# Performance work log

Measured on AMD Instinct MI355X. Metric: run time of the kernel, lower is better.

Reference implementation:

```python
import jax, jax.numpy as jnp
import numpy as np

N = 8192      # nodes
IN_FEATS = 128
OUT_FEATS = 64
DEG = 16      # avg degree for random edges
NEG_SLOPE = 0.01  # nn.LeakyReLU default


def setup_inputs() -> dict:
    key = jax.random.key(0)
    k1, k2, k3, k4, k5, k6 = jax.random.split(key, 6)
    inputs = jax.random.normal(k1, (N, IN_FEATS), dtype=jnp.float32)
    # Random symmetric adjacency with self-loops (dense, as in the original module)
    us = jax.random.randint(k2, (N * DEG,), 0, N)
    vs = jax.random.randint(k3, (N * DEG,), 0, N)
    A = jnp.zeros((N, N), dtype=jnp.float32)
    A = A.at[us, vs].set(1.0)
    A = A.at[vs, us].set(1.0)
    idx = jnp.arange(N)
    A = A.at[idx, idx].set(1.0)
    # Linear layer params (torch nn.Linear: weight [out, in])
    W = jax.random.normal(k4, (OUT_FEATS, IN_FEATS), dtype=jnp.float32) * (1.0 / np.sqrt(IN_FEATS))
    b = jnp.zeros((OUT_FEATS,), dtype=jnp.float32)
    # attention params, torch.rand -> uniform [0,1)
    a1 = jax.random.uniform(k5, (1, OUT_FEATS), dtype=jnp.float32)
    a2 = jax.random.uniform(k6, (1, OUT_FEATS), dtype=jnp.float32)
    return {"inputs": inputs, "A": A, "W": W, "b": b, "a1": a1, "a2": a2}


def reference(inputs, A, W, b, a1, a2):
    z = inputs @ W.T + b                                  # [N, out]
    zi = jnp.sum(a1 * z, axis=1, keepdims=True)           # [N, 1]
    zj = jnp.sum(a2 * z, axis=1, keepdims=True)           # [N, 1]
    n = A.shape[0]
    idx = jnp.arange(n)
    diagA = jnp.diagonal(A)                               # A_ii
    # attention_A + attention_B = A*zi + diag(A_ii * zj)  (A*(eye*zj) only keeps diagonal)
    att = A * zi
    att = att.at[idx, idx].add(diagA * zj[:, 0])
    att = jax.nn.leaky_relu(att, NEG_SLOPE)
    att = jnp.exp(att) * A
    att = att / jnp.sum(att, axis=1, keepdims=True)       # row-normalize
    h = z - att @ z
    return jax.nn.relu(h)
```

## Files before the change

kernel.cpp:

```cpp
#include <hip/hip_runtime.h>
#include <math.h>

#define NN 8192
#define IN_F 128
#define OUT_F 64
#define NEG_SLOPE 0.01f
#define K1_ROWS 8
#define CAP 256

typedef int v4i __attribute__((ext_vector_type(4)));

__global__ __launch_bounds__(256, 4) void k1_linear(
    const float* __restrict__ X, const float* __restrict__ W,
    const float* __restrict__ b, const float* __restrict__ a1,
    const float* __restrict__ a2, float* __restrict__ z,
    float* __restrict__ ev, float* __restrict__ dv)
{
    __shared__ float Wl[OUT_F * 129];
    __shared__ float xs[K1_ROWS * IN_F];
    const int t = threadIdx.x;
    const int blk = blockIdx.x;

    for (int idx = t; idx < OUT_F * IN_F; idx += 256) {
        int f = idx >> 7, k = idx & 127;
        Wl[f * 129 + k] = W[idx];
    }
    {
        const float4* Xv = reinterpret_cast<const float4*>(X + (size_t)blk * (K1_ROWS * IN_F));
        float4* xsv = reinterpret_cast<float4*>(xs);
        if (t < K1_ROWS * IN_F / 4) xsv[t] = Xv[t];
    }
    __syncthreads();

    const int wid = t >> 6;
    const int lane = t & 63;
    const float bias = b[lane];
    const float a1f = a1[lane], a2f = a2[lane];

#pragma unroll
    for (int r2 = 0; r2 < 2; ++r2) {
        const int row = wid * 2 + r2;
        float acc = 0.f;
#pragma unroll 8
        for (int k = 0; k < IN_F; ++k)
            acc = fmaf(xs[row * IN_F + k], Wl[lane * 129 + k], acc);
        const float zval = acc + bias;
        const int i = blk * K1_ROWS + row;
        z[i * OUT_F + lane] = zval;

        float p1 = a1f * zval;
        float p2 = a2f * zval;
#pragma unroll
        for (int off = 32; off > 0; off >>= 1) {
            p1 += __shfl_down(p1, off, 64);
            p2 += __shfl_down(p2, off, 64);
        }
        if (lane == 0) {
            const float s1 = p1;
            const float s2 = p1 + p2;
            const float l1 = s1 > 0.f ? s1 : NEG_SLOPE * s1;
            const float l2 = s2 > 0.f ? s2 : NEG_SLOPE * s2;
            ev[i] = expf(l1);
            dv[i] = expf(l2);
        }
    }
}

__global__ __launch_bounds__(256, 8) void k2_fused(
    const float* __restrict__ A, const float* __restrict__ z,
    const float* __restrict__ ev, const float* __restrict__ dv,
    float* __restrict__ out)
{
    __shared__ int lst[CAP];
    __shared__ int cnt;
    __shared__ float accw[4][64];

    const int i = blockIdx.x;
    const int t = threadIdx.x;
    const int wid = t >> 6, lane = t & 63;

    if (t == 0) cnt = 0;
    __syncthreads();

    const v4i* __restrict__ Arow = reinterpret_cast<const v4i*>(A + (size_t)i * NN);

    v4i b0 = __builtin_nontemporal_load(&Arow[0 * 256 + t]);
    v4i b1 = __builtin_nontemporal_load(&Arow[1 * 256 + t]);
    v4i b2 = __builtin_nontemporal_load(&Arow[2 * 256 + t]);
    v4i b3 = __builtin_nontemporal_load(&Arow[3 * 256 + t]);
    v4i b4 = __builtin_nontemporal_load(&Arow[4 * 256 + t]);
    v4i b5 = __builtin_nontemporal_load(&Arow[5 * 256 + t]);
    v4i b6 = __builtin_nontemporal_load(&Arow[6 * 256 + t]);
    v4i b7 = __builtin_nontemporal_load(&Arow[7 * 256 + t]);

#define STEP(S, B)                                                              \
    {                                                                           \
        const int base = ((S) * 256 + t) * 4;                                   \
        if (B.x != 0) { int k = atomicAdd(&cnt, 1); if (k < CAP) lst[k] = base;     } \
        if (B.y != 0) { int k = atomicAdd(&cnt, 1); if (k < CAP) lst[k] = base + 1; } \
        if (B.z != 0) { int k = atomicAdd(&cnt, 1); if (k < CAP) lst[k] = base + 2; } \
        if (B.w != 0) { int k = atomicAdd(&cnt, 1); if (k < CAP) lst[k] = base + 3; } \
    }
    STEP(0, b0) STEP(1, b1) STEP(2, b2) STEP(3, b3)
    STEP(4, b4) STEP(5, b5) STEP(6, b6) STEP(7, b7)
#undef STEP

    __syncthreads();
    const int c0 = cnt;
    const int c = c0 < CAP ? c0 : CAP;

    float acc = 0.f;
    {
        int k = wid;
        for (; k + 4 < c; k += 8) {
            const int j0 = lst[k];
            const int j1 = lst[k + 4];
            const float z0 = z[(size_t)j0 * OUT_F + lane];
            const float z1 = z[(size_t)j1 * OUT_F + lane];
            acc += z0 + z1;
        }
        if (k < c)
            acc += z[(size_t)lst[k] * OUT_F + lane];
    }
    accw[wid][lane] = acc;
    __syncthreads();

    if (wid == 0) {
        const float sumNbr = accw[0][lane] + accw[1][lane]
                           + accw[2][lane] + accw[3][lane];
        const float degT = (float)c0;
        const float e = ev[i], d = dv[i];
        const float S = (degT - 1.f) * e + d;
        const float zif = z[(size_t)i * OUT_F + lane];
        const float h = zif * (1.f + (e - d) / S) - (e / S) * sumNbr;
        out[(size_t)i * OUT_F + lane] = h > 0.f ? h : 0.f;
    }
}

extern "C" void kernel_launch(void* const* d_in, const int* in_sizes, int n_in,
                              void* d_out, int out_size, void* d_ws, size_t ws_size,
                              hipStream_t stream) {
    const float* X  = (const float*)d_in[0];
    const float* A  = (const float*)d_in[1];
    const float* W  = (const float*)d_in[2];
    const float* b  = (const float*)d_in[3];
    const float* a1 = (const float*)d_in[4];
    const float* a2 = (const float*)d_in[5];
    float* out = (float*)d_out;

    float* ws = (float*)d_ws;
    float* z  = ws;
    float* ev = ws + NN * OUT_F;
    float* dv = ev + NN;

    k1_linear<<<NN / K1_ROWS, 256, 0, stream>>>(X, W, b, a1, a2, z, ev, dv);
    k2_fused<<<NN, 256, 0, stream>>>(A, z, ev, dv, out);
}
```

Before: 61.78 us.

## Fuse linear projection into the attention kernel by aggregating raw input neighbors

Drops the separate linear-layer kernel and the z/ev/dv workspace. Each row block now gathers and sums neighbor rows of X (128 floats each) instead of z rows, then applies W to both its own row and the neighbor sum. It recomputes the attention scalars in-block, relying on the bias cancelling out of the final expression. This removes one launch and the round trip of z through memory, at the cost of gathering twice as many bytes per neighbor and every block re-reading the full 32KB W from cache.

```diff
diff --git a/kernel.cpp b/kernel.cpp
--- a/kernel.cpp
+++ b/kernel.cpp
@@ -5,85 +5,30 @@
 #define IN_F 128
 #define OUT_F 64
 #define NEG_SLOPE 0.01f
-#define K1_ROWS 8
 #define CAP 256
 
 typedef int v4i __attribute__((ext_vector_type(4)));
 
-__global__ __launch_bounds__(256, 4) void k1_linear(
-    const float* __restrict__ X, const float* __restrict__ W,
-    const float* __restrict__ b, const float* __restrict__ a1,
-    const float* __restrict__ a2, float* __restrict__ z,
-    float* __restrict__ ev, float* __restrict__ dv)
-{
-    __shared__ float Wl[OUT_F * 129];
-    __shared__ float xs[K1_ROWS * IN_F];
-    const int t = threadIdx.x;
-    const int blk = blockIdx.x;
-
-    for (int idx = t; idx < OUT_F * IN_F; idx += 256) {
-        int f = idx >> 7, k = idx & 127;
-        Wl[f * 129 + k] = W[idx];
-    }
-    {
-        const float4* Xv = reinterpret_cast<const float4*>(X + (size_t)blk * (K1_ROWS * IN_F));
-        float4* xsv = reinterpret_cast<float4*>(xs);
-        if (t < K1_ROWS * IN_F / 4) xsv[t] = Xv[t];
-    }
-    __syncthreads();
-
-    const int wid = t >> 6;
-    const int lane = t & 63;
-    const float bias = b[lane];
-    const float a1f = a1[lane], a2f = a2[lane];
-
-#pragma unroll
-    for (int r2 = 0; r2 < 2; ++r2) {
-        const int row = wid * 2 + r2;
-        float acc = 0.f;
-#pragma unroll 8
-        for (int k = 0; k < IN_F; ++k)
-            acc = fmaf(xs[row * IN_F + k], Wl[lane * 129 + k], acc);
-        const float zval = acc + bias;
-        const int i = blk * K1_ROWS + row;
-        z[i * OUT_F + lane] = zval;
-
-        float p1 = a1f * zval;
-        float p2 = a2f * zval;
-#pragma unroll
-        for (int off = 32; off > 0; off >>= 1) {
-            p1 += __shfl_down(p1, off, 64);
-            p2 += __shfl_down(p2, off, 64);
-        }
-        if (lane == 0) {
-            const float s1 = p1;
-            const float s2 = p1 + p2;
-            const float l1 = s1 > 0.f ? s1 : NEG_SLOPE * s1;
-            const float l2 = s2 > 0.f ? s2 : NEG_SLOPE * s2;
-            ev[i] = expf(l1);
-            dv[i] = expf(l2);
-        }
-    }
-}
-
-__global__ __launch_bounds__(256, 8) void k2_fused(
-    const float* __restrict__ A, const float* __restrict__ z,
-    const float* __restrict__ ev, const float* __restrict__ dv,
+__global__ __launch_bounds__(256, 8) void aagnn_fused(
+    const float* __restrict__ A, const float* __restrict__ X,
+    const float* __restrict__ W, const float* __restrict__ b,
+    const float* __restrict__ a1, const float* __restrict__ a2,
     float* __restrict__ out)
 {
-    __shared__ int lst[CAP];
-    __shared__ int cnt;
-    __shared__ float accw[4][64];
+    __shared__ float xs[IN_F];
+    __shared__ float sx[2][IN_F];
+    __shared__ int   lst[CAP];
+    __shared__ int   cnt;
+    __shared__ float po[OUT_F], pog[OUT_F];
 
     const int i = blockIdx.x;
     const int t = threadIdx.x;
-    const int wid = t >> 6, lane = t & 63;
 
-    if (t == 0) cnt = 0;
-    __syncthreads();
+    float4 xv = {0.f, 0.f, 0.f, 0.f};
+    if (t < 32)
+        xv = reinterpret_cast<const float4*>(X + (size_t)i * IN_F)[t];
 
     const v4i* __restrict__ Arow = reinterpret_cast<const v4i*>(A + (size_t)i * NN);
-
     v4i b0 = __builtin_nontemporal_load(&Arow[0 * 256 + t]);
     v4i b1 = __builtin_nontemporal_load(&Arow[1 * 256 + t]);
     v4i b2 = __builtin_nontemporal_load(&Arow[2 * 256 + t]);
@@ -92,6 +37,10 @@
     v4i b5 = __builtin_nontemporal_load(&Arow[5 * 256 + t]);
     v4i b6 = __builtin_nontemporal_load(&Arow[6 * 256 + t]);
     v4i b7 = __builtin_nontemporal_load(&Arow[7 * 256 + t]);
+
+    if (t == 0) cnt = 0;
+    if (t < 32) reinterpret_cast<float4*>(xs)[t] = xv;
+    __syncthreads();
 
 #define STEP(S, B)                                                              \
     {                                                                           \
@@ -109,31 +58,72 @@
     const int c0 = cnt;
     const int c = c0 < CAP ? c0 : CAP;
 
-    float acc = 0.f;
     {
-        int k = wid;
-        for (; k + 4 < c; k += 8) {
-            const int j0 = lst[k];
-            const int j1 = lst[k + 4];
-            const float z0 = z[(size_t)j0 * OUT_F + lane];
-            const float z1 = z[(size_t)j1 * OUT_F + lane];
-            acc += z0 + z1;
+        const int h = t >> 7, k = t & 127;
+        float acc = 0.f;
+        int e = h;
+        for (; e + 6 < c; e += 8) {
+            const int j0 = lst[e],     j1 = lst[e + 2];
+            const int j2 = lst[e + 4], j3 = lst[e + 6];
+            const float v0 = X[(size_t)j0 * IN_F + k];
+            const float v1 = X[(size_t)j1 * IN_F + k];
+            const float v2 = X[(size_t)j2 * IN_F + k];
+            const float v3 = X[(size_t)j3 * IN_F + k];
+            acc += (v0 + v1) + (v2 + v3);
         }
-        if (k < c)
-            acc += z[(size_t)lst[k] * OUT_F + lane];
+        for (; e < c; e += 2)
+            acc += X[(size_t)lst[e] * IN_F + k];
+        sx[h][k] = acc;
     }
-    accw[wid][lane] = acc;
     __syncthreads();
 
-    if (wid == 0) {
-        const float sumNbr = accw[0][lane] + accw[1][lane]
-                           + accw[2][lane] + accw[3][lane];
-        const float degT = (float)c0;
-        const float e = ev[i], d = dv[i];
-        const float S = (degT - 1.f) * e + d;
-        const float zif = z[(size_t)i * OUT_F + lane];
-        const float h = zif * (1.f + (e - d) / S) - (e / S) * sumNbr;
-        out[(size_t)i * OUT_F + lane] = h > 0.f ? h : 0.f;
+    float u = 0.f, g = 0.f;
+    {
+        const float4* Wv = reinterpret_cast<const float4*>(W) + (size_t)t * 8;
+#pragma unroll
+        for (int q = 0; q < 8; ++q) {
+            const float4 w4 = Wv[q];
+            const int base = (t & 3) * 32 + q * 4;
+            const float x0 = xs[base + 0], x1 = xs[base + 1];
+            const float x2 = xs[base + 2], x3 = xs[base + 3];
+            const float s0 = sx[0][base + 0] + sx[1][base + 0];
+            const float s1 = sx[0][base + 1] + sx[1][base + 1];
+            const float s2 = sx[0][base + 2] + sx[1][base + 2];
+            const float s3 = sx[0][base + 3] + sx[1][base + 3];
+            u = fmaf(w4.x, x0, u); u = fmaf(w4.y, x1, u);
+            u = fmaf(w4.z, x2, u); u = fmaf(w4.w, x3, u);
+            g = fmaf(w4.x, s0, g); g = fmaf(w4.y, s1, g);
+            g = fmaf(w4.z, s2, g); g = fmaf(w4.w, s3, g);
+        }
+    }
+    u += __shfl_xor(u, 1, 64); u += __shfl_xor(u, 2, 64);
+    g += __shfl_xor(g, 1, 64); g += __shfl_xor(g, 2, 64);
+    if ((t & 3) == 0) { po[t >> 2] = u; pog[t >> 2] = g; }
+    __syncthreads();
+
+    if (t < 64) {
+        const float zv = po[t];
+        const float gv = pog[t];
+        const float bf = b[t];
+        float p1 = a1[t] * (zv + bf);
+        float p2 = a2[t] * (zv + bf);
+#pragma unroll
+        for (int off = 32; off > 0; off >>= 1) {
+            p1 += __shfl_down(p1, off, 64);
+            p2 += __shfl_down(p2, off, 64);
+        }
+        const float zi = p1, zj = p2;
+        const float l1 = zi > 0.f ? zi : NEG_SLOPE * zi;
+        const float s2v = zi + zj;
+        const float l2 = s2v > 0.f ? s2v : NEG_SLOPE * s2v;
+        const float ee = expf(l1), dd = expf(l2);
+        const float S = ((float)c0 - 1.f) * ee + dd;
+        float alpha = 1.f + (ee - dd) / S;
+        float beta  = ee / S;
+        alpha = __shfl(alpha, 0, 64);
+        beta  = __shfl(beta, 0, 64);
+        const float hv = alpha * zv - beta * gv;
+        out[(size_t)i * OUT_F + t] = hv > 0.f ? hv : 0.f;
     }
 }
 
@@ -148,11 +138,5 @@
     const float* a2 = (const float*)d_in[5];
     float* out = (float*)d_out;
 
-    float* ws = (float*)d_ws;
-    float* z  = ws;
-    float* ev = ws + NN * OUT_F;
-    float* dv = ev + NN;
-
-    k1_linear<<<NN / K1_ROWS, 256, 0, stream>>>(X, W, b, a1, a2, z, ev, dv);
-    k2_fused<<<NN, 256, 0, stream>>>(A, z, ev, dv, out);
+    aagnn_fused<<<NN, 256, 0, stream>>>(A, X, W, b, a1, a2, out);
 }
```

New measurement: 88.89 us. +43.9%, slower.
